# Kernel tuning notes

Measured on AMD Instinct MI355X. Metric: run time of the kernel, lower is better.

Reference implementation:

```python
import jax, jax.numpy as jnp
import numpy as np


def _make_cameras(key, B):
    """Well-conditioned c = [cam2world(16), intrinsics(9)] per batch."""
    k1, k2 = jax.random.split(key)
    # random rotation via Gram-Schmidt on a random 3x3
    A = jax.random.normal(k1, (B, 3, 3), dtype=jnp.float32)
    q0 = A[:, :, 0] / jnp.linalg.norm(A[:, :, 0], axis=-1, keepdims=True)
    v1 = A[:, :, 1] - jnp.sum(A[:, :, 1] * q0, -1, keepdims=True) * q0
    q1 = v1 / jnp.linalg.norm(v1, axis=-1, keepdims=True)
    q2 = jnp.cross(q0, q1)
    R = jnp.stack([q0, q1, q2], axis=-1)                      # [B,3,3]
    t = 2.7 * q2                                              # camera at radius 2.7 along view axis
    cam2world = jnp.zeros((B, 4, 4), jnp.float32)
    cam2world = cam2world.at[:, :3, :3].set(R)
    cam2world = cam2world.at[:, :3, 3].set(t)
    cam2world = cam2world.at[:, 3, 3].set(1.0)
    # EG3D-style normalized intrinsics: fx=fy=4.2647, cx=cy=0.5, sk=0
    intr = jnp.tile(jnp.array([[4.2647, 0.0, 0.5],
                               [0.0, 4.2647, 0.5],
                               [0.0, 0.0, 1.0]], jnp.float32), (B, 1, 1))
    return jnp.concatenate([cam2world.reshape(B, 16), intr.reshape(B, 9)], axis=1)


def setup_inputs() -> dict:
    key = jax.random.key(0)
    kc, kd, kp = jax.random.split(key, 3)
    B, R, M = 8, 64, 4096
    c = _make_cameras(kc, B)
    image_depth = 2.2 + 1.1 * jax.random.uniform(kd, (B, R * R, 1), dtype=jnp.float32)
    pc = 0.3 * jax.random.normal(kp, (B, M, 3), dtype=jnp.float32)
    return {"c": c, "image_depth": image_depth, "pc": pc, "resolution": R}


def _ray_sampler(cam2world, intrinsics, resolution):
    B = cam2world.shape[0]
    N = resolution * resolution
    fx = intrinsics[:, 0, 0][:, None]
    fy = intrinsics[:, 1, 1][:, None]
    cx = intrinsics[:, 0, 2][:, None]
    cy = intrinsics[:, 1, 2][:, None]
    sk = intrinsics[:, 0, 1][:, None]
    r = (jnp.arange(resolution, dtype=jnp.float32) + 0.5) / resolution
    gi, gj = jnp.meshgrid(r, r, indexing='ij')                # row, col
    x_cam = jnp.broadcast_to(gj.reshape(-1), (B, N))          # uv.flip(0): x is col coord
    y_cam = jnp.broadcast_to(gi.reshape(-1), (B, N))
    z_cam = jnp.ones((B, N), jnp.float32)
    x_lift = (x_cam - cx + cy * sk / fy - sk * y_cam / fy) / fx * z_cam
    y_lift = (y_cam - cy) / fy * z_cam
    cam_rel = jnp.stack([x_lift, y_lift, z_cam, jnp.ones_like(z_cam)], axis=-1)  # [B,N,4]
    world = jnp.einsum('bij,bnj->bni', cam2world, cam_rel)[..., :3]
    origins = cam2world[:, :3, 3]                              # [B,3]
    dirs = world - origins[:, None, :]
    dirs = dirs / jnp.linalg.norm(dirs, axis=-1, keepdims=True)
    ray_origins = jnp.broadcast_to(origins[:, None, :], dirs.shape)
    return ray_origins, dirs


def _chamfer(x, y):
    # squared-distance NN both directions; GEMM-form pairwise distances
    x2 = jnp.sum(x * x, axis=-1)                               # [B,N]
    y2 = jnp.sum(y * y, axis=-1)                               # [B,M]
    xy = jnp.einsum('bnd,bmd->bnm', x, y)                      # [B,N,M]
    d = x2[:, :, None] + y2[:, None, :] - 2.0 * xy
    return jnp.min(d, axis=2), jnp.min(d, axis=1)              # dist1 [B,N], dist2 [B,M]


def reference(c, image_depth, pc, resolution):
    B = c.shape[0]
    pc = pc[..., :3]
    depth = image_depth.reshape(B, -1, 1)
    cam2world = c[:, :16].reshape(-1, 4, 4)
    intr = c[:, 16:25].reshape(-1, 3, 3)
    ro, rd = _ray_sampler(cam2world, intr, resolution)
    pred_pos = depth * rd + ro                                  # [B,N,3]
    d0, d1 = _chamfer(pred_pos, pc)
    K = min(pred_pos.shape[1], pc.shape[1]) // 2
    d0s = jnp.sort(d0, axis=1)[:, :K]
    d1s = d0s  # NOTE: faithful to original code (loss_1_sorted is assigned from loss_0_sorted)
    loss0 = jnp.mean(d0s, axis=1)
    loss1 = jnp.mean(d1s, axis=1)
    return (loss0 + loss1).reshape(B, 1)
```

## Files before the change

kernel.cpp:

```cpp
#include <hip/hip_runtime.h>
#include <math.h>

#define FLT_BIG 3.0e38f
#define HIST_BINS 16384

__global__ __launch_bounds__(256, 2) void chamfer_min_kernel(
    const float* __restrict__ cparam,
    const float* __restrict__ depth,
    const float* __restrict__ pc,
    float* __restrict__ d0,
    int N, int M, int R)
{
    const int b   = blockIdx.y;
    const int tid = threadIdx.x;

    extern __shared__ float4 s4[];

    const float* pcb = pc + (size_t)b * M * 3;
    for (int idx = tid; idx < M; idx += 256) {
        float x = pcb[idx * 3 + 0];
        float y = pcb[idx * 3 + 1];
        float z = pcb[idx * 3 + 2];
        s4[idx] = make_float4(x, y, z, 0.5f * (x * x + y * y + z * z));
    }
    __syncthreads();

    const float* cb = cparam + (size_t)b * 25;
    const float fx = cb[16], sk = cb[17], cx = cb[18];
    const float fy = cb[20], cy = cb[21];

    const int chunk = tid & 31;
    const int grp   = tid >> 5;
    const int nbase = blockIdx.x * 64 + grp * 8;

    const int i0 = nbase / R;
    const int j0 = nbase - i0 * R;
    const float y_cam = (i0 + 0.5f) / (float)R;
    const float y_lift = (y_cam - cy) / fy;
    const float base_x = (-cx + cy * sk / fy - sk * y_cam / fy);

    float px[8], py[8], pz[8], e[8];
    #pragma unroll
    for (int r = 0; r < 8; r++) {
        const float x_cam = (j0 + r + 0.5f) / (float)R;
        const float x_lift = (x_cam + base_x) / fx;
        const float dxw = cb[0] * x_lift + cb[1] * y_lift + cb[2];
        const float dyw = cb[4] * x_lift + cb[5] * y_lift + cb[6];
        const float dzw = cb[8] * x_lift + cb[9] * y_lift + cb[10];
        const float inv = 1.0f / sqrtf(dxw * dxw + dyw * dyw + dzw * dzw);
        const float dep = depth[(size_t)b * N + nbase + r];
        px[r] = cb[3]  + dep * dxw * inv;
        py[r] = cb[7]  + dep * dyw * inv;
        pz[r] = cb[11] + dep * dzw * inv;
        e[r]  = FLT_BIG;
    }

    const int Mc = M >> 5;
    for (int m = 0; m < Mc; m += 8) {
        float4 q[8];
        #pragma unroll
        for (int mm = 0; mm < 8; mm++)
            q[mm] = s4[((m + mm) << 5) + chunk];
        #pragma unroll
        for (int mm = 0; mm < 8; mm++) {
            #pragma unroll
            for (int r = 0; r < 8; r++) {
                float t = fmaf(-px[r], q[mm].x, q[mm].w);
                t = fmaf(-py[r], q[mm].y, t);
                t = fmaf(-pz[r], q[mm].z, t);
                e[r] = fminf(e[r], t);
            }
        }
    }

    #pragma unroll
    for (int r = 0; r < 8; r++) {
        float v = e[r];
        v = fminf(v, __shfl_xor(v, 1));
        v = fminf(v, __shfl_xor(v, 2));
        v = fminf(v, __shfl_xor(v, 4));
        v = fminf(v, __shfl_xor(v, 8));
        v = fminf(v, __shfl_xor(v, 16));
        e[r] = v;
    }
    if (chunk == 0) {
        #pragma unroll
        for (int r = 0; r < 8; r++) {
            const float pn = px[r] * px[r] + py[r] * py[r] + pz[r] * pz[r];
            d0[(size_t)b * N + nbase + r] = fmaxf(2.0f * e[r] + pn, 0.0f);
        }
    }
}

__global__ __launch_bounds__(256, 1) void select_mean_kernel(
    const float* __restrict__ d0,
    float* __restrict__ out,
    int N, int K)
{
    const int b   = blockIdx.x;
    const int tid = threadIdx.x;

    extern __shared__ unsigned int hist[];
    __shared__ unsigned int spart[256];
    __shared__ unsigned int s_selbin, s_krem;
    __shared__ unsigned int subcnt[32];
    __shared__ float        subsum[32];
    __shared__ float        s_below;

    for (int t2 = tid; t2 < HIST_BINS; t2 += 256) hist[t2] = 0u;
    if (tid < 32) { subcnt[tid] = 0u; subsum[tid] = 0.0f; }
    if (tid == 0) s_below = 0.0f;
    __syncthreads();

    unsigned int key[16];
    #pragma unroll
    for (int t2 = 0; t2 < 16; t2++)
        key[t2] = __float_as_uint(d0[(size_t)b * N + t2 * 256 + tid]);
    #pragma unroll
    for (int t2 = 0; t2 < 16; t2++)
        atomicAdd(&hist[key[t2] >> 18], 1u);
    __syncthreads();

    unsigned int psum = 0u;
    #pragma unroll 8
    for (int i2 = 0; i2 < 64; i2++)
        psum += hist[(tid << 6) + ((i2 + tid) & 63)];
    spart[tid] = psum;
    __syncthreads();

    unsigned int cbef = 0u;
    for (int i2 = 0; i2 < tid; i2++) cbef += spart[i2];
    if (cbef < (unsigned int)K && (unsigned int)K <= cbef + psum) {
        unsigned int k2 = (unsigned int)K - cbef;
        unsigned int sel = 0u;
        for (int i2 = 0; i2 < 64; i2++) {
            unsigned int h = hist[(tid << 6) + i2];
            if (k2 <= h) { sel = (tid << 6) + i2; break; }
            k2 -= h;
        }
        s_selbin = sel;
        s_krem   = k2;
    }
    __syncthreads();

    const unsigned int selbin = s_selbin;
    float sumb = 0.0f;
    #pragma unroll
    for (int t2 = 0; t2 < 16; t2++) {
        const unsigned int bin = key[t2] >> 18;
        const float v = __uint_as_float(key[t2]);
        if (bin < selbin) sumb += v;
        if (bin == selbin) {
            const unsigned int sub = (key[t2] >> 13) & 31u;
            atomicAdd(&subcnt[sub], 1u);
            atomicAdd(&subsum[sub], v);
        }
    }
    atomicAdd(&s_below, sumb);
    __syncthreads();

    if (tid == 0) {
        unsigned int k2 = s_krem;
        float s = s_below;
        for (int i2 = 0; i2 < 32; i2++) {
            unsigned int h = subcnt[i2];
            if (k2 <= h) {
                s += (h ? (subsum[i2] * ((float)k2 / (float)h)) : 0.0f);
                break;
            }
            s += subsum[i2];
            k2 -= h;
        }
        out[b] = 2.0f * s / (float)K;
    }
}

extern "C" void kernel_launch(void* const* d_in, const int* in_sizes, int n_in,
                              void* d_out, int out_size, void* d_ws, size_t ws_size,
                              hipStream_t stream)
{
    const float* c   = (const float*)d_in[0];
    const float* dep = (const float*)d_in[1];
    const float* pc  = (const float*)d_in[2];
    float* out = (float*)d_out;

    const int B = in_sizes[0] / 25;
    const int N = in_sizes[1] / B;
    const int M = in_sizes[2] / (3 * B);
    int R = 1; while (R * R < N) R++;

    float* d0 = (float*)d_ws;

    dim3 gridA(N / 64, B);
    size_t ldsA = (size_t)M * sizeof(float4);
    hipLaunchKernelGGL(chamfer_min_kernel, gridA, dim3(256), ldsA, stream,
                       c, dep, pc, d0, N, M, R);

    const int K = ((N < M) ? N : M) / 2;
    size_t ldsB = (size_t)HIST_BINS * sizeof(unsigned int);
    hipLaunchKernelGGL(select_mean_kernel, dim3(B), dim3(256), ldsB, stream,
                       d0, out, N, K);
}
```

Before: 88.11 us.

## Compute chamfer pairwise distances with bf16 MFMA instead of scalar FMAs

```diff
diff --git a/kernel.cpp b/kernel.cpp
--- a/kernel.cpp
+++ b/kernel.cpp
@@ -4,24 +4,49 @@
 #define FLT_BIG 3.0e38f
 #define HIST_BINS 16384
 
-__global__ __launch_bounds__(256, 2) void chamfer_min_kernel(
+typedef short short8 __attribute__((ext_vector_type(8)));
+typedef float floatx4 __attribute__((ext_vector_type(4)));
+
+union U4S8 { uint4 u; short8 s; };
+
+static __device__ __forceinline__ unsigned int f2bf(float f) {
+    unsigned int u = __float_as_uint(f);
+    return (u + 0x7FFFu + ((u >> 16) & 1u)) >> 16;
+}
+static __device__ __forceinline__ float bf2f(unsigned int b) {
+    return __uint_as_float(b << 16);
+}
+
+__global__ __launch_bounds__(256, 2) void chamfer_mfma_kernel(
     const float* __restrict__ cparam,
     const float* __restrict__ depth,
     const float* __restrict__ pc,
     float* __restrict__ d0,
     int N, int M, int R)
 {
-    const int b   = blockIdx.y;
-    const int tid = threadIdx.x;
-
-    extern __shared__ float4 s4[];
+    const int b    = blockIdx.y;
+    const int tid  = threadIdx.x;
+    const int lane = tid & 63;
+    const int wave = tid >> 6;
+    const int m16  = lane & 15;
+    const int quad = lane >> 4;
+
+    extern __shared__ uint4 sld[];
 
     const float* pcb = pc + (size_t)b * M * 3;
-    for (int idx = tid; idx < M; idx += 256) {
-        float x = pcb[idx * 3 + 0];
-        float y = pcb[idx * 3 + 1];
-        float z = pcb[idx * 3 + 2];
-        s4[idx] = make_float4(x, y, z, 0.5f * (x * x + y * y + z * z));
+    const int Ms = M >> 8;
+    for (int s = 0; s < Ms; s++) {
+        const int idx = s * 256 + tid;
+        const float x = pcb[idx * 3 + 0];
+        const float y = pcb[idx * 3 + 1];
+        const float z = pcb[idx * 3 + 2];
+        const float hq = 0.5f * (x * x + y * y + z * z);
+        uint4 u;
+        u.x = f2bf(x) | (f2bf(y) << 16);
+        u.y = f2bf(z) | (f2bf(hq) << 16);
+        u.z = 0x3F803F80u;
+        u.w = 0u;
+        sld[idx] = u;
     }
     __syncthreads();
 
@@ -29,66 +54,71 @@
     const float fx = cb[16], sk = cb[17], cx = cb[18];
     const float fy = cb[20], cy = cb[21];
 
-    const int chunk = tid & 31;
-    const int grp   = tid >> 5;
-    const int nbase = blockIdx.x * 64 + grp * 8;
-
-    const int i0 = nbase / R;
-    const int j0 = nbase - i0 * R;
+    const int nbase = blockIdx.x * 64 + wave * 16;
+    const int n  = nbase + m16;
+    const int i0 = n / R;
+    const int j0 = n - i0 * R;
+    const float x_cam = (j0 + 0.5f) / (float)R;
     const float y_cam = (i0 + 0.5f) / (float)R;
+    const float x_lift = (x_cam - cx + cy * sk / fy - sk * y_cam / fy) / fx;
     const float y_lift = (y_cam - cy) / fy;
-    const float base_x = (-cx + cy * sk / fy - sk * y_cam / fy);
-
-    float px[8], py[8], pz[8], e[8];
-    #pragma unroll
-    for (int r = 0; r < 8; r++) {
-        const float x_cam = (j0 + r + 0.5f) / (float)R;
-        const float x_lift = (x_cam + base_x) / fx;
-        const float dxw = cb[0] * x_lift + cb[1] * y_lift + cb[2];
-        const float dyw = cb[4] * x_lift + cb[5] * y_lift + cb[6];
-        const float dzw = cb[8] * x_lift + cb[9] * y_lift + cb[10];
-        const float inv = 1.0f / sqrtf(dxw * dxw + dyw * dyw + dzw * dzw);
-        const float dep = depth[(size_t)b * N + nbase + r];
-        px[r] = cb[3]  + dep * dxw * inv;
-        py[r] = cb[7]  + dep * dyw * inv;
-        pz[r] = cb[11] + dep * dzw * inv;
-        e[r]  = FLT_BIG;
-    }
-
-    const int Mc = M >> 5;
-    for (int m = 0; m < Mc; m += 8) {
-        float4 q[8];
+    const float dxw = cb[0] * x_lift + cb[1] * y_lift + cb[2];
+    const float dyw = cb[4] * x_lift + cb[5] * y_lift + cb[6];
+    const float dzw = cb[8] * x_lift + cb[9] * y_lift + cb[10];
+    const float inv = 1.0f / sqrtf(dxw * dxw + dyw * dyw + dzw * dzw);
+    const float dep = depth[(size_t)b * N + n];
+    const float px = cb[3]  + dep * dxw * inv;
+    const float py = cb[7]  + dep * dyw * inv;
+    const float pz = cb[11] + dep * dzw * inv;
+
+    const float hp = 0.5f * (px * px + py * py + pz * pz);
+    const unsigned int hp_hi = f2bf(hp);
+    const unsigned int hp_lo = f2bf(hp - bf2f(hp_hi));
+
+    U4S8 af;
+    af.u = make_uint4(0u, 0u, 0u, 0u);
+    if (quad == 0) {
+        af.u.x = f2bf(-px) | (f2bf(-py) << 16);
+        af.u.y = f2bf(-pz) | (0x3F80u << 16);
+        af.u.z = hp_hi | (hp_lo << 16);
+        af.u.w = 0u;
+    }
+    const short8 afrag = af.s;
+    const floatx4 zero4 = {0.0f, 0.0f, 0.0f, 0.0f};
+
+    floatx4 mins = {FLT_BIG, FLT_BIG, FLT_BIG, FLT_BIG};
+
+    const int T = M >> 4;
+    for (int m = 0; m < T; m += 8) {
+        uint4 bu[8];
         #pragma unroll
         for (int mm = 0; mm < 8; mm++)
-            q[mm] = s4[((m + mm) << 5) + chunk];
+            bu[mm] = sld[((m + mm) << 4) + m16];
         #pragma unroll
         for (int mm = 0; mm < 8; mm++) {
-            #pragma unroll
-            for (int r = 0; r < 8; r++) {
-                float t = fmaf(-px[r], q[mm].x, q[mm].w);
-                t = fmaf(-py[r], q[mm].y, t);
-                t = fmaf(-pz[r], q[mm].z, t);
-                e[r] = fminf(e[r], t);
-            }
-        }
-    }
-
-    #pragma unroll
-    for (int r = 0; r < 8; r++) {
-        float v = e[r];
+            U4S8 bf; bf.u = bu[mm];
+            floatx4 d = __builtin_amdgcn_mfma_f32_16x16x32_bf16(
+                            afrag, bf.s, zero4, 0, 0, 0);
+            mins[0] = fminf(mins[0], d[0]);
+            mins[1] = fminf(mins[1], d[1]);
+            mins[2] = fminf(mins[2], d[2]);
+            mins[3] = fminf(mins[3], d[3]);
+        }
+    }
+
+    float dv[4];
+    #pragma unroll
+    for (int t = 0; t < 4; t++) {
+        float v = mins[t];
         v = fminf(v, __shfl_xor(v, 1));
         v = fminf(v, __shfl_xor(v, 2));
         v = fminf(v, __shfl_xor(v, 4));
         v = fminf(v, __shfl_xor(v, 8));
-        v = fminf(v, __shfl_xor(v, 16));
-        e[r] = v;
-    }
-    if (chunk == 0) {
-        #pragma unroll
-        for (int r = 0; r < 8; r++) {
-            const float pn = px[r] * px[r] + py[r] * py[r] + pz[r] * pz[r];
-            d0[(size_t)b * N + nbase + r] = fmaxf(2.0f * e[r] + pn, 0.0f);
-        }
+        dv[t] = fmaxf(2.0f * v, 0.0f);
+    }
+    if (m16 == 0) {
+        float4* o = (float4*)(d0 + (size_t)b * N + nbase + quad * 4);
+        *o = make_float4(dv[0], dv[1], dv[2], dv[3]);
     }
 }
 
@@ -192,8 +222,8 @@
     float* d0 = (float*)d_ws;
 
     dim3 gridA(N / 64, B);
-    size_t ldsA = (size_t)M * sizeof(float4);
-    hipLaunchKernelGGL(chamfer_min_kernel, gridA, dim3(256), ldsA, stream,
+    size_t ldsA = (size_t)M * sizeof(uint4);
+    hipLaunchKernelGGL(chamfer_mfma_kernel, gridA, dim3(256), ldsA, stream,
                        c, dep, pc, d0, N, M, R);
 
     const int K = ((N < M) ? N : M) / 2;
```

New measurement: 81.85 us. 7.1% less time.
